# Kernel optimization log

Measured on AMD Instinct MI355X. Metric: run time of the kernel, lower is better.

The kernel has to match this reference:

```python
import jax, jax.numpy as jnp
import numpy as np

N_NODES = 50000
N_EDGES = 1600000
IN_CH, HID_CH, OUT_CH = 128, 128, 64


def gcn_conv(x, src, dst, norm, W, b):
    # x: [N, d_in]; src/dst: [E'] (self-loops included); norm: [E']
    h = x @ W                                  # [N, d_out] transform first (dense GEMM)
    msg = h[src] * norm[:, None]               # [E', d_out] gather + scale
    out = jax.ops.segment_sum(msg, dst, num_segments=x.shape[0])  # scatter-add
    return out + b


def setup_inputs() -> dict:
    key = jax.random.key(0)
    k1, k2, k3, k4, k5, k6 = jax.random.split(key, 6)
    x = jax.random.normal(k1, (N_NODES, IN_CH), dtype=jnp.float32)
    edge_index = jax.random.randint(k2, (2, N_EDGES), 0, N_NODES, dtype=jnp.int64)
    # Glorot-style init for weights
    W1 = jax.random.normal(k3, (IN_CH, HID_CH), dtype=jnp.float32) / np.sqrt(IN_CH)
    b1 = jnp.zeros((HID_CH,), dtype=jnp.float32)
    W2 = jax.random.normal(k4, (HID_CH, OUT_CH), dtype=jnp.float32) / np.sqrt(HID_CH)
    b2 = jnp.zeros((OUT_CH,), dtype=jnp.float32)
    return {"x": x, "edge_index": edge_index, "W1": W1, "b1": b1, "W2": W2, "b2": b2}


def reference(x, edge_index, W1, b1, W2, b2):
    n = x.shape[0]
    # GCNConv default: add self-loops, symmetric normalization D^-1/2 (A+I) D^-1/2
    loop = jnp.arange(n, dtype=edge_index.dtype)
    src = jnp.concatenate([edge_index[0], loop])   # [E+N]
    dst = jnp.concatenate([edge_index[1], loop])   # [E+N]
    deg = jax.ops.segment_sum(jnp.ones_like(dst, dtype=x.dtype), dst, num_segments=n)
    dinv = jnp.where(deg > 0, jax.lax.rsqrt(deg), 0.0)  # [N]
    norm = dinv[src] * dinv[dst]                   # [E+N]

    h = gcn_conv(x, src, dst, norm, W1, b1)        # conv1
    h = jax.nn.relu(h)
    h = gcn_conv(h, src, dst, norm, W2, b2)        # conv2
    return jax.nn.log_softmax(h, axis=1)
```

## Files before the change

kernel.cpp:

```cpp
#include <hip/hip_runtime.h>
#include <hip/hip_bf16.h>
#include <math.h>


typedef unsigned int uint;
typedef unsigned short ushort_t;
typedef unsigned char uchar_t;
typedef __attribute__((ext_vector_type(8))) short bf16x8;
typedef __attribute__((ext_vector_type(4))) float f32x4;
typedef __attribute__((ext_vector_type(2))) float f32x2;

#define BSH 7
#define NBMAX 400
#define BIN_CHUNK 4096
#define CAP 6144

__device__ inline ushort_t f2b(float f) {
    uint u = __float_as_uint(f);
    return (ushort_t)((u + 0x7fffu + ((u >> 16) & 1u)) >> 16);
}

__device__ inline uchar_t f2e4m3_sw(float f) {
    float a = fabsf(f);
    a = fminf(a, 448.f);
    uint sign = (__float_as_uint(f) >> 24) & 0x80u;
    uint u = __float_as_uint(a);
    int e = (int)(u >> 23) - 127;
    uint code;
    if (e < -6) {
        float t = a * 512.0f;
        uint m = (uint)(t + 0.5f);
        code = (m > 7) ? 0x08u : m;
    } else {
        uint lsb = (u >> 20) & 1u;
        u += 0x0007FFFFu + lsb;
        e = (int)(u >> 23) - 127;
        if (e > 8) code = 0x7Eu;
        else code = ((uint)(e + 7) << 3) | ((u >> 20) & 7u);
    }
    return (uchar_t)(sign | code);
}
__device__ inline float e4m3_sw(uint c) {
    uint ef = (c >> 3) & 15u, m = c & 7u;
    float v = ef ? __uint_as_float(((ef + 120u) << 23) | (m << 20))
                 : (float)m * 0.001953125f;
    return (c & 0x80u) ? -v : v;
}

__device__ inline f32x2 fp8x2_f32(uint v) {
#if __has_builtin(__builtin_amdgcn_cvt_pk_f32_fp8)
    return __builtin_amdgcn_cvt_pk_f32_fp8(v, false);
#else
    return (f32x2){e4m3_sw(v & 255u), e4m3_sw((v >> 8) & 255u)};
#endif
}
__device__ inline float fp8_f32(uint v) {
#if __has_builtin(__builtin_amdgcn_cvt_f32_fp8)
    return __builtin_amdgcn_cvt_f32_fp8(v, 0);
#else
    return e4m3_sw(v & 255u);
#endif
}
__device__ inline uchar_t f32_fp8(float f) {
#if __has_builtin(__builtin_amdgcn_cvt_pk_fp8_f32)
    return (uchar_t)(__builtin_amdgcn_cvt_pk_fp8_f32(f, f, 0u, false) & 0xffu);
#else
    return f2e4m3_sw(f);
#endif
}

__global__ __launch_bounds__(256) void k_init(int* __restrict__ bktcnt, int nbk) {
    int i = blockIdx.x * 256 + threadIdx.x;
    if (i < nbk) bktcnt[i] = 0;
}

__global__ __launch_bounds__(256) void k_bin(const int* __restrict__ esrc, const int* __restrict__ edst,
                                             int* __restrict__ bktcnt, uint* __restrict__ bin,
                                             int e, int nbk) {
    __shared__ int hist[NBMAX];
    __shared__ int segbase[NBMAX];
    int tid = threadIdx.x;
    int b0 = blockIdx.x * BIN_CHUNK;
    int b1 = min(b0 + BIN_CHUNK, e);
    for (int i = tid; i < nbk; i += 256) hist[i] = 0;
    __syncthreads();
    for (int i = b0 + tid * 4; i < b1; i += 1024) {
        if (i + 4 <= b1) {
            int4 d = *(const int4*)&edst[i];
            atomicAdd(&hist[d.x >> BSH], 1);
            atomicAdd(&hist[d.y >> BSH], 1);
            atomicAdd(&hist[d.z >> BSH], 1);
            atomicAdd(&hist[d.w >> BSH], 1);
        } else {
            for (int j = i; j < b1; ++j) atomicAdd(&hist[edst[j] >> BSH], 1);
        }
    }
    __syncthreads();
    for (int b = tid; b < nbk; b += 256) {
        int c = hist[b];
        int gb = c ? atomicAdd(&bktcnt[b], c) : 0;
        segbase[b] = b * CAP + gb;
        hist[b] = 0;
    }
    __syncthreads();
    for (int i = b0 + tid * 4; i < b1; i += 1024) {
        if (i + 4 <= b1) {
            int4 d = *(const int4*)&edst[i];
            int4 s = *(const int4*)&esrc[i];
            int bx = d.x >> BSH, by = d.y >> BSH, bz = d.z >> BSH, bw = d.w >> BSH;
            int px = atomicAdd(&hist[bx], 1);
            int py = atomicAdd(&hist[by], 1);
            int pz = atomicAdd(&hist[bz], 1);
            int pw = atomicAdd(&hist[bw], 1);
            bin[segbase[bx] + px] = (uint)s.x | ((uint)(d.x & 127) << 17);
            bin[segbase[by] + py] = (uint)s.y | ((uint)(d.y & 127) << 17);
            bin[segbase[bz] + pz] = (uint)s.z | ((uint)(d.z & 127) << 17);
            bin[segbase[bw] + pw] = (uint)s.w | ((uint)(d.w & 127) << 17);
        } else {
            for (int j = i; j < b1; ++j) {
                int d = edst[j], s = esrc[j];
                int b = d >> BSH;
                int p = atomicAdd(&hist[b], 1);
                bin[segbase[b] + p] = (uint)s | ((uint)(d & 127) << 17);
            }
        }
    }
}

__global__ __launch_bounds__(512) void k_scanBkt(const int* __restrict__ bktcnt, int* __restrict__ bktoff,
                                                 int nbk) {
    int tid = threadIdx.x;
    int v = (tid < nbk) ? bktcnt[tid] : 0;
    int x = v;
    for (int off = 1; off < 64; off <<= 1) {
        int y = __shfl_up(x, off);
        if ((tid & 63) >= off) x += y;
    }
    __shared__ int wt[8];
    if ((tid & 63) == 63) wt[tid >> 6] = x;
    __syncthreads();
    int w = tid >> 6, woff = 0;
    for (int k = 0; k < w; ++k) woff += wt[k];
    if (tid < nbk) bktoff[tid] = x - v + woff;
}

__global__ __launch_bounds__(256) void k_bucket(const uint* __restrict__ bin, const int* __restrict__ bktcnt,
                                                const int* __restrict__ bktoff,
                                                int* __restrict__ rowstart, int* __restrict__ cnt,
                                                float* __restrict__ dinv, int* __restrict__ csr, int n) {
    __shared__ int lcnt[1 << BSH];
    __shared__ int cur[1 << BSH];
    __shared__ int wt[4];
    int b = blockIdx.x;
    int tid = threadIdx.x;
    int lo = b << BSH;
    int nl = min(1 << BSH, n - lo);
    int m = bktcnt[b];
    int base = b * CAP;
    int obase = bktoff[b];
    if (tid < (1 << BSH)) lcnt[tid] = 0;
    __syncthreads();
    for (int i = tid; i < m; i += 256) {
        uint v = bin[base + i];
        atomicAdd(&lcnt[v >> 17], 1);
    }
    __syncthreads();
    int v = (tid < (1 << BSH)) ? lcnt[tid] : 0;
    int x = v;
    for (int off = 1; off < 64; off <<= 1) {
        int y = __shfl_up(x, off);
        if ((tid & 63) >= off) x += y;
    }
    if ((tid & 63) == 63) wt[tid >> 6] = x;
    __syncthreads();
    int excl = x - v + ((tid >= 64 && tid < 128) ? wt[0] : 0);
    if (tid < nl) {
        int node = lo + tid;
        rowstart[node] = obase + excl;
        cnt[node] = v;
        dinv[node] = rsqrtf((float)(v + 1));
        cur[tid] = obase + excl;
    }
    __syncthreads();
    for (int i = tid; i < m; i += 256) {
        uint en = bin[base + i];
        int dl = en >> 17;
        int p = atomicAdd(&cur[dl], 1);
        csr[p] = (int)(en & 0x1FFFFu);
    }
}

__global__ __launch_bounds__(256) void k_cvtW(const float* __restrict__ W1, const float* __restrict__ W2,
                                              ushort_t* __restrict__ W1t, ushort_t* __restrict__ W2t) {
    int i = blockIdx.x * 256 + threadIdx.x;
    if (i < 16384) {
        int k = i >> 7, nn = i & 127;
        W1t[nn * 128 + k] = f2b(W1[k * 128 + nn]);
    } else if (i < 16384 + 8192) {
        int j = i - 16384;
        int k = j >> 6, nn = j & 63;
        W2t[nn * 128 + k] = f2b(W2[k * 64 + nn]);
    }
}

template <int COLS, bool XBF16, bool OUTFP8>
__global__ __launch_bounds__(256) void k_mgemm(const void* __restrict__ Xv, const ushort_t* __restrict__ Wt,
                                               void* __restrict__ Yv, int nrows) {
    constexpr int NT = COLS / 16;
    __shared__ ushort_t lsX[64 * 128];
    __shared__ ushort_t lsW[COLS * 128];
    int tid = threadIdx.x;
    int rbase = blockIdx.x * 64;

#pragma unroll
    for (int it = 0; it < 4; ++it) {
        int idx = (tid + it * 256) * 8;
        int r = idx >> 7, c = idx & 127;
        int grow = rbase + r;
        uint4 pv = make_uint4(0, 0, 0, 0);
        if (grow < nrows) {
            if (XBF16) {
                pv = *(const uint4*)((const ushort_t*)Xv + (size_t)grow * 128 + c);
            } else {
                const float* xp = (const float*)Xv + (size_t)grow * 128 + c;
                float4 a = *(const float4*)xp;
                float4 b = *(const float4*)(xp + 4);
                pv.x = (uint)f2b(a.x) | ((uint)f2b(a.y) << 16);
                pv.y = (uint)f2b(a.z) | ((uint)f2b(a.w) << 16);
                pv.z = (uint)f2b(b.x) | ((uint)f2b(b.y) << 16);
                pv.w = (uint)f2b(b.z) | ((uint)f2b(b.w) << 16);
            }
        }
        int boff = (r * 256 + c * 2) ^ ((r & 7) << 4);
        *(uint4*)((char*)lsX + boff) = pv;
    }
#pragma unroll
    for (int it = 0; it < NT; ++it) {
        int idx = (tid + it * 256) * 8;
        int nr = idx >> 7, k = idx & 127;
        uint4 v = *(const uint4*)&Wt[nr * 128 + k];
        int boff = (nr * 256 + k * 2) ^ ((nr & 7) << 4);
        *(uint4*)((char*)lsW + boff) = v;
    }
    __syncthreads();

    int w = tid >> 6, l = tid & 63;
    int lr = l & 15, lg = l >> 4;
    int xrow = w * 16 + lr;
    bf16x8 a[4];
#pragma unroll
    for (int ks = 0; ks < 4; ++ks) {
        int boff = (xrow * 256 + (ks * 32 + lg * 8) * 2) ^ ((xrow & 7) << 4);
        a[ks] = *(const bf16x8*)((const char*)lsX + boff);
    }
    f32x4 acc[NT];
#pragma unroll
    for (int ct = 0; ct < NT; ++ct) {
        acc[ct] = (f32x4){0.f, 0.f, 0.f, 0.f};
#pragma unroll
        for (int ks = 0; ks < 4; ++ks) {
            int wrow = ct * 16 + lr;
            int boff = (wrow * 256 + (ks * 32 + lg * 8) * 2) ^ ((wrow & 7) << 4);
            bf16x8 b = *(const bf16x8*)((const char*)lsW + boff);
            acc[ct] = __builtin_amdgcn_mfma_f32_16x16x32_bf16(a[ks], b, acc[ct], 0, 0, 0);
        }
    }
#pragma unroll
    for (int ct = 0; ct < NT; ++ct) {
        int ch = ct * 16 + lr;
#pragma unroll
        for (int r = 0; r < 4; ++r) {
            int row = rbase + w * 16 + lg * 4 + r;
            if (row < nrows) {
                if (OUTFP8) ((uchar_t*)Yv)[(size_t)row * COLS + ch] = f32_fp8(acc[ct][r]);
                else        ((ushort_t*)Yv)[(size_t)row * COLS + ch] = f2b(acc[ct][r]);
            }
        }
    }
}

__global__ __launch_bounds__(256) void k_agg1(const ushort_t* __restrict__ xw8,
                                              const int* __restrict__ csr,
                                              const int* __restrict__ rowstart, const int* __restrict__ cnt,
                                              const float* __restrict__ dinv, const float* __restrict__ b1,
                                              uint* __restrict__ h, int n) {
    int tid = threadIdx.x;
    int i = blockIdx.x * 4 + (tid >> 6);
    int lane = tid & 63;
    if (i >= n) return;
    float di = dinv[i];
    f32x2 sv = fp8x2_f32(xw8[((uint)i << 6) + lane]);
    float accx = sv.x * di, accy = sv.y * di;
    int beg = rowstart[i], m = cnt[i];
    int j = 0;
    for (; j + 8 <= m; j += 8) {
        int s0 = csr[beg + j + 0], s1 = csr[beg + j + 1], s2 = csr[beg + j + 2], s3 = csr[beg + j + 3];
        int s4 = csr[beg + j + 4], s5 = csr[beg + j + 5], s6 = csr[beg + j + 6], s7 = csr[beg + j + 7];
        float d0 = dinv[s0], d1 = dinv[s1], d2 = dinv[s2], d3 = dinv[s3];
        float d4 = dinv[s4], d5 = dinv[s5], d6 = dinv[s6], d7 = dinv[s7];
        uint v0 = xw8[((uint)s0 << 6) + lane];
        uint v1 = xw8[((uint)s1 << 6) + lane];
        uint v2 = xw8[((uint)s2 << 6) + lane];
        uint v3 = xw8[((uint)s3 << 6) + lane];
        uint v4 = xw8[((uint)s4 << 6) + lane];
        uint v5 = xw8[((uint)s5 << 6) + lane];
        uint v6 = xw8[((uint)s6 << 6) + lane];
        uint v7 = xw8[((uint)s7 << 6) + lane];
        f32x2 f0 = fp8x2_f32(v0), f1 = fp8x2_f32(v1), f2 = fp8x2_f32(v2), f3 = fp8x2_f32(v3);
        f32x2 f4 = fp8x2_f32(v4), f5 = fp8x2_f32(v5), f6 = fp8x2_f32(v6), f7 = fp8x2_f32(v7);
        accx = fmaf(d0, f0.x, accx); accy = fmaf(d0, f0.y, accy);
        accx = fmaf(d1, f1.x, accx); accy = fmaf(d1, f1.y, accy);
        accx = fmaf(d2, f2.x, accx); accy = fmaf(d2, f2.y, accy);
        accx = fmaf(d3, f3.x, accx); accy = fmaf(d3, f3.y, accy);
        accx = fmaf(d4, f4.x, accx); accy = fmaf(d4, f4.y, accy);
        accx = fmaf(d5, f5.x, accx); accy = fmaf(d5, f5.y, accy);
        accx = fmaf(d6, f6.x, accx); accy = fmaf(d6, f6.y, accy);
        accx = fmaf(d7, f7.x, accx); accy = fmaf(d7, f7.y, accy);
    }
    for (; j < m; ++j) {
        int s0 = csr[beg + j];
        float d0 = dinv[s0];
        f32x2 f0 = fp8x2_f32(xw8[((uint)s0 << 6) + lane]);
        accx = fmaf(d0, f0.x, accx); accy = fmaf(d0, f0.y, accy);
    }
    float2 bb = ((const float2*)b1)[lane];
    float ox = fmaxf(fmaf(di, accx, bb.x), 0.f);
    float oy = fmaxf(fmaf(di, accy, bb.y), 0.f);
    h[((uint)i << 6) + lane] = (uint)f2b(ox) | ((uint)f2b(oy) << 16);
}

__global__ __launch_bounds__(256) void k_agg2(const uchar_t* __restrict__ hw8,
                                              const int* __restrict__ csr,
                                              const int* __restrict__ rowstart, const int* __restrict__ cnt,
                                              const float* __restrict__ dinv, const float* __restrict__ b2,
                                              float* __restrict__ out, int n) {
    int tid = threadIdx.x;
    int i = blockIdx.x * 4 + (tid >> 6);
    int lane = tid & 63;
    if (i >= n) return;
    float di = dinv[i];
    float acc = fp8_f32(hw8[((uint)i << 6) + lane]) * di;
    int beg = rowstart[i], m = cnt[i];
    int j = 0;
    for (; j + 8 <= m; j += 8) {
        int s0 = csr[beg + j + 0], s1 = csr[beg + j + 1], s2 = csr[beg + j + 2], s3 = csr[beg + j + 3];
        int s4 = csr[beg + j + 4], s5 = csr[beg + j + 5], s6 = csr[beg + j + 6], s7 = csr[beg + j + 7];
        float d0 = dinv[s0], d1 = dinv[s1], d2 = dinv[s2], d3 = dinv[s3];
        float d4 = dinv[s4], d5 = dinv[s5], d6 = dinv[s6], d7 = dinv[s7];
        uint c0 = hw8[((uint)s0 << 6) + lane];
        uint c1 = hw8[((uint)s1 << 6) + lane];
        uint c2 = hw8[((uint)s2 << 6) + lane];
        uint c3 = hw8[((uint)s3 << 6) + lane];
        uint c4 = hw8[((uint)s4 << 6) + lane];
        uint c5 = hw8[((uint)s5 << 6) + lane];
        uint c6 = hw8[((uint)s6 << 6) + lane];
        uint c7 = hw8[((uint)s7 << 6) + lane];
        acc = fmaf(d0, fp8_f32(c0), acc);
        acc = fmaf(d1, fp8_f32(c1), acc);
        acc = fmaf(d2, fp8_f32(c2), acc);
        acc = fmaf(d3, fp8_f32(c3), acc);
        acc = fmaf(d4, fp8_f32(c4), acc);
        acc = fmaf(d5, fp8_f32(c5), acc);
        acc = fmaf(d6, fp8_f32(c6), acc);
        acc = fmaf(d7, fp8_f32(c7), acc);
    }
    for (; j < m; ++j) {
        int s0 = csr[beg + j];
        acc = fmaf(dinv[s0], fp8_f32((uint)hw8[((uint)s0 << 6) + lane]), acc);
    }
    float o = fmaf(di, acc, b2[lane]);
    float mx = o;
    for (int off = 32; off; off >>= 1) mx = fmaxf(mx, __shfl_xor(mx, off));
    float ex = expf(o - mx);
    float sum = ex;
    for (int off = 32; off; off >>= 1) sum += __shfl_xor(sum, off);
    out[((uint)i << 6) + lane] = o - mx - logf(sum);
}

extern "C" void kernel_launch(void* const* d_in, const int* in_sizes, int n_in,
                              void* d_out, int out_size, void* d_ws, size_t ws_size,
                              hipStream_t stream) {
    const float* x  = (const float*)d_in[0];
    const int* eidx = (const int*)d_in[1];
    const float* W1 = (const float*)d_in[2];
    const float* b1 = (const float*)d_in[3];
    const float* W2 = (const float*)d_in[4];
    const float* b2 = (const float*)d_in[5];
    float* out = (float*)d_out;

    const int n = in_sizes[0] / 128;
    const int e = in_sizes[1] / 2;
    const int* esrc = eidx;
    const int* edst = eidx + e;
    const int nbk = (n + (1 << BSH) - 1) >> BSH;

    size_t off = 0;
    auto carve = [&](size_t bytes) {
        void* p = (char*)d_ws + off;
        off += (bytes + 255) & ~(size_t)255;
        return p;
    };
    uchar_t*  xW1  = (uchar_t*)carve((size_t)n * 128);
    ushort_t* h    = (ushort_t*)carve((size_t)n * 128 * 2);
    uchar_t*  hW2  = (uchar_t*)carve((size_t)n * 64);
    ushort_t* W1t  = (ushort_t*)carve(128 * 128 * 2);
    ushort_t* W2t  = (ushort_t*)carve(64 * 128 * 2);
    int*   cnt     = (int*)carve((size_t)n * 4);
    float* dinv    = (float*)carve((size_t)n * 4);
    int*   rowstart= (int*)carve((size_t)n * 4);
    int*   bktcnt  = (int*)carve((size_t)nbk * 4);
    int*   bktoff  = (int*)carve((size_t)nbk * 4);
    uint*  bin     = (uint*)carve((size_t)nbk * CAP * 4);
    int*   csr     = (int*)carve((size_t)e * 4);
    (void)ws_size;

    const int nbBin  = (e + BIN_CHUNK - 1) / BIN_CHUNK;
    const int nbWave = (n + 3) / 4;
    const int nbGemm = (n + 63) / 64;

    k_init<<<(nbk + 255) / 256, 256, 0, stream>>>(bktcnt, nbk);
    k_bin<<<nbBin, 256, 0, stream>>>(esrc, edst, bktcnt, bin, e, nbk);
    k_scanBkt<<<1, 512, 0, stream>>>(bktcnt, bktoff, nbk);
    k_bucket<<<nbk, 256, 0, stream>>>(bin, bktcnt, bktoff, rowstart, cnt, dinv, csr, n);
    k_cvtW<<<96, 256, 0, stream>>>(W1, W2, W1t, W2t);

    k_mgemm<128, false, true><<<nbGemm, 256, 0, stream>>>(x, W1t, xW1, n);
    k_agg1<<<nbWave, 256, 0, stream>>>((const ushort_t*)xW1, csr, rowstart, cnt, dinv, b1, (uint*)h, n);

    k_mgemm<64, true, true><<<nbGemm, 256, 0, stream>>>(h, W2t, hW2, n);
    k_agg2<<<nbWave, 256, 0, stream>>>(hW2, csr, rowstart, cnt, dinv, b2, out, n);
}
```

Baseline: 161.6 us.

## Prescale GEMM outputs by dinv and split edges across wave halves in aggregation

The GEMM epilogue now multiplies each output row by dinv[row] before quantizing to FP8. This removes the per-edge dinv[src] gather and FMA from both aggregation kernels, which become plain adds. The aggregation kernels are restructured so each lane loads 4 FP8 bytes at once. Edges are split across wave halves (layer 1) or quarters (layer 2), with neighbor indices broadcast via shuffles and partial sums combined by xor-shuffles. The log-softmax reduction is also narrowed to 16 lanes with float4 stores. Prescaling before FP8 quantization slightly changes rounding behaviour.

```diff
diff --git a/kernel.cpp b/kernel.cpp
--- a/kernel.cpp
+++ b/kernel.cpp
@@ -47,18 +47,18 @@
     return (c & 0x80u) ? -v : v;
 }
 
-__device__ inline f32x2 fp8x2_f32(uint v) {
+__device__ inline f32x2 fp8x2_lo(uint v) {
 #if __has_builtin(__builtin_amdgcn_cvt_pk_f32_fp8)
     return __builtin_amdgcn_cvt_pk_f32_fp8(v, false);
 #else
     return (f32x2){e4m3_sw(v & 255u), e4m3_sw((v >> 8) & 255u)};
 #endif
 }
-__device__ inline float fp8_f32(uint v) {
-#if __has_builtin(__builtin_amdgcn_cvt_f32_fp8)
-    return __builtin_amdgcn_cvt_f32_fp8(v, 0);
+__device__ inline f32x2 fp8x2_hi(uint v) {
+#if __has_builtin(__builtin_amdgcn_cvt_pk_f32_fp8)
+    return __builtin_amdgcn_cvt_pk_f32_fp8(v, true);
 #else
-    return e4m3_sw(v & 255u);
+    return (f32x2){e4m3_sw((v >> 16) & 255u), e4m3_sw((v >> 24) & 255u)};
 #endif
 }
 __device__ inline uchar_t f32_fp8(float f) {
@@ -205,6 +205,7 @@
 
 template <int COLS, bool XBF16, bool OUTFP8>
 __global__ __launch_bounds__(256) void k_mgemm(const void* __restrict__ Xv, const ushort_t* __restrict__ Wt,
+                                               const float* __restrict__ dinv,
                                                void* __restrict__ Yv, int nrows) {
     constexpr int NT = COLS / 16;
     __shared__ ushort_t lsX[64 * 128];
@@ -265,6 +266,12 @@
             acc[ct] = __builtin_amdgcn_mfma_f32_16x16x32_bf16(a[ks], b, acc[ct], 0, 0, 0);
         }
     }
+    float dr[4];
+#pragma unroll
+    for (int r = 0; r < 4; ++r) {
+        int row = rbase + w * 16 + lg * 4 + r;
+        dr[r] = (OUTFP8 && row < nrows) ? dinv[row] : 1.f;
+    }
 #pragma unroll
     for (int ct = 0; ct < NT; ++ct) {
         int ch = ct * 16 + lr;
@@ -272,109 +279,136 @@
         for (int r = 0; r < 4; ++r) {
             int row = rbase + w * 16 + lg * 4 + r;
             if (row < nrows) {
-                if (OUTFP8) ((uchar_t*)Yv)[(size_t)row * COLS + ch] = f32_fp8(acc[ct][r]);
+                if (OUTFP8) ((uchar_t*)Yv)[(size_t)row * COLS + ch] = f32_fp8(dr[r] * acc[ct][r]);
                 else        ((ushort_t*)Yv)[(size_t)row * COLS + ch] = f2b(acc[ct][r]);
             }
         }
     }
 }
 
-__global__ __launch_bounds__(256) void k_agg1(const ushort_t* __restrict__ xw8,
+__global__ __launch_bounds__(256) void k_agg1(const uchar_t* __restrict__ t1,
                                               const int* __restrict__ csr,
                                               const int* __restrict__ rowstart, const int* __restrict__ cnt,
                                               const float* __restrict__ dinv, const float* __restrict__ b1,
                                               uint* __restrict__ h, int n) {
     int tid = threadIdx.x;
     int i = blockIdx.x * 4 + (tid >> 6);
+    if (i >= n) return;
     int lane = tid & 63;
-    if (i >= n) return;
-    float di = dinv[i];
-    f32x2 sv = fp8x2_f32(xw8[((uint)i << 6) + lane]);
-    float accx = sv.x * di, accy = sv.y * di;
+    int half = lane >> 5, cl = lane & 31;
+    float a0 = 0.f, a1 = 0.f, a2 = 0.f, a3 = 0.f;
+    if (half == 0) {
+        uint v = *(const uint*)(t1 + ((size_t)i << 7) + cl * 4);
+        f32x2 lo = fp8x2_lo(v), hi = fp8x2_hi(v);
+        a0 = lo.x; a1 = lo.y; a2 = hi.x; a3 = hi.y;
+    }
     int beg = rowstart[i], m = cnt[i];
     int j = 0;
     for (; j + 8 <= m; j += 8) {
-        int s0 = csr[beg + j + 0], s1 = csr[beg + j + 1], s2 = csr[beg + j + 2], s3 = csr[beg + j + 3];
-        int s4 = csr[beg + j + 4], s5 = csr[beg + j + 5], s6 = csr[beg + j + 6], s7 = csr[beg + j + 7];
-        float d0 = dinv[s0], d1 = dinv[s1], d2 = dinv[s2], d3 = dinv[s3];
-        float d4 = dinv[s4], d5 = dinv[s5], d6 = dinv[s6], d7 = dinv[s7];
-        uint v0 = xw8[((uint)s0 << 6) + lane];
-        uint v1 = xw8[((uint)s1 << 6) + lane];
-        uint v2 = xw8[((uint)s2 << 6) + lane];
-        uint v3 = xw8[((uint)s3 << 6) + lane];
-        uint v4 = xw8[((uint)s4 << 6) + lane];
-        uint v5 = xw8[((uint)s5 << 6) + lane];
-        uint v6 = xw8[((uint)s6 << 6) + lane];
-        uint v7 = xw8[((uint)s7 << 6) + lane];
-        f32x2 f0 = fp8x2_f32(v0), f1 = fp8x2_f32(v1), f2 = fp8x2_f32(v2), f3 = fp8x2_f32(v3);
-        f32x2 f4 = fp8x2_f32(v4), f5 = fp8x2_f32(v5), f6 = fp8x2_f32(v6), f7 = fp8x2_f32(v7);
-        accx = fmaf(d0, f0.x, accx); accy = fmaf(d0, f0.y, accy);
-        accx = fmaf(d1, f1.x, accx); accy = fmaf(d1, f1.y, accy);
-        accx = fmaf(d2, f2.x, accx); accy = fmaf(d2, f2.y, accy);
-        accx = fmaf(d3, f3.x, accx); accy = fmaf(d3, f3.y, accy);
-        accx = fmaf(d4, f4.x, accx); accy = fmaf(d4, f4.y, accy);
-        accx = fmaf(d5, f5.x, accx); accy = fmaf(d5, f5.y, accy);
-        accx = fmaf(d6, f6.x, accx); accy = fmaf(d6, f6.y, accy);
-        accx = fmaf(d7, f7.x, accx); accy = fmaf(d7, f7.y, accy);
-    }
-    for (; j < m; ++j) {
-        int s0 = csr[beg + j];
-        float d0 = dinv[s0];
-        f32x2 f0 = fp8x2_f32(xw8[((uint)s0 << 6) + lane]);
-        accx = fmaf(d0, f0.x, accx); accy = fmaf(d0, f0.y, accy);
-    }
-    float2 bb = ((const float2*)b1)[lane];
-    float ox = fmaxf(fmaf(di, accx, bb.x), 0.f);
-    float oy = fmaxf(fmaf(di, accy, bb.y), 0.f);
-    h[((uint)i << 6) + lane] = (uint)f2b(ox) | ((uint)f2b(oy) << 16);
-}
-
-__global__ __launch_bounds__(256) void k_agg2(const uchar_t* __restrict__ hw8,
+        int c = csr[beg + j + (lane & 7)];
+        int s0 = __shfl(c, 0 + half);
+        int s1 = __shfl(c, 2 + half);
+        int s2 = __shfl(c, 4 + half);
+        int s3 = __shfl(c, 6 + half);
+        uint v0 = *(const uint*)(t1 + ((size_t)s0 << 7) + cl * 4);
+        uint v1 = *(const uint*)(t1 + ((size_t)s1 << 7) + cl * 4);
+        uint v2 = *(const uint*)(t1 + ((size_t)s2 << 7) + cl * 4);
+        uint v3 = *(const uint*)(t1 + ((size_t)s3 << 7) + cl * 4);
+        f32x2 p;
+        p = fp8x2_lo(v0); a0 += p.x; a1 += p.y;  p = fp8x2_hi(v0); a2 += p.x; a3 += p.y;
+        p = fp8x2_lo(v1); a0 += p.x; a1 += p.y;  p = fp8x2_hi(v1); a2 += p.x; a3 += p.y;
+        p = fp8x2_lo(v2); a0 += p.x; a1 += p.y;  p = fp8x2_hi(v2); a2 += p.x; a3 += p.y;
+        p = fp8x2_lo(v3); a0 += p.x; a1 += p.y;  p = fp8x2_hi(v3); a2 += p.x; a3 += p.y;
+    }
+    for (; j < m; j += 2) {
+        int idx = j + half;
+        if (idx < m) {
+            int s = csr[beg + idx];
+            uint v = *(const uint*)(t1 + ((size_t)s << 7) + cl * 4);
+            f32x2 p;
+            p = fp8x2_lo(v); a0 += p.x; a1 += p.y;
+            p = fp8x2_hi(v); a2 += p.x; a3 += p.y;
+        }
+    }
+    a0 += __shfl_xor(a0, 32); a1 += __shfl_xor(a1, 32);
+    a2 += __shfl_xor(a2, 32); a3 += __shfl_xor(a3, 32);
+    float di = dinv[i];
+    float4 bb = ((const float4*)b1)[cl];
+    float o0 = fmaxf(fmaf(di, a0, bb.x), 0.f);
+    float o1 = fmaxf(fmaf(di, a1, bb.y), 0.f);
+    float o2 = fmaxf(fmaf(di, a2, bb.z), 0.f);
+    float o3 = fmaxf(fmaf(di, a3, bb.w), 0.f);
+    if (half == 0) {
+        uint2 pk;
+        pk.x = (uint)f2b(o0) | ((uint)f2b(o1) << 16);
+        pk.y = (uint)f2b(o2) | ((uint)f2b(o3) << 16);
+        *(uint2*)&h[((size_t)i << 6) + cl * 2] = pk;
+    }
+}
+
+__global__ __launch_bounds__(256) void k_agg2(const uchar_t* __restrict__ t2,
                                               const int* __restrict__ csr,
                                               const int* __restrict__ rowstart, const int* __restrict__ cnt,
                                               const float* __restrict__ dinv, const float* __restrict__ b2,
                                               float* __restrict__ out, int n) {
     int tid = threadIdx.x;
     int i = blockIdx.x * 4 + (tid >> 6);
+    if (i >= n) return;
     int lane = tid & 63;
-    if (i >= n) return;
-    float di = dinv[i];
-    float acc = fp8_f32(hw8[((uint)i << 6) + lane]) * di;
+    int q = lane >> 4, cl = lane & 15;
+    float a0 = 0.f, a1 = 0.f, a2 = 0.f, a3 = 0.f;
+    if (q == 0) {
+        uint v = *(const uint*)(t2 + ((size_t)i << 6) + cl * 4);
+        f32x2 lo = fp8x2_lo(v), hi = fp8x2_hi(v);
+        a0 = lo.x; a1 = lo.y; a2 = hi.x; a3 = hi.y;
+    }
     int beg = rowstart[i], m = cnt[i];
     int j = 0;
     for (; j + 8 <= m; j += 8) {
-        int s0 = csr[beg + j + 0], s1 = csr[beg + j + 1], s2 = csr[beg + j + 2], s3 = csr[beg + j + 3];
-        int s4 = csr[beg + j + 4], s5 = csr[beg + j + 5], s6 = csr[beg + j + 6], s7 = csr[beg + j + 7];
-        float d0 = dinv[s0], d1 = dinv[s1], d2 = dinv[s2], d3 = dinv[s3];
-        float d4 = dinv[s4], d5 = dinv[s5], d6 = dinv[s6], d7 = dinv[s7];
-        uint c0 = hw8[((uint)s0 << 6) + lane];
-        uint c1 = hw8[((uint)s1 << 6) + lane];
-        uint c2 = hw8[((uint)s2 << 6) + lane];
-        uint c3 = hw8[((uint)s3 << 6) + lane];
-        uint c4 = hw8[((uint)s4 << 6) + lane];
-        uint c5 = hw8[((uint)s5 << 6) + lane];
-        uint c6 = hw8[((uint)s6 << 6) + lane];
-        uint c7 = hw8[((uint)s7 << 6) + lane];
-        acc = fmaf(d0, fp8_f32(c0), acc);
-        acc = fmaf(d1, fp8_f32(c1), acc);
-        acc = fmaf(d2, fp8_f32(c2), acc);
-        acc = fmaf(d3, fp8_f32(c3), acc);
-        acc = fmaf(d4, fp8_f32(c4), acc);
-        acc = fmaf(d5, fp8_f32(c5), acc);
-        acc = fmaf(d6, fp8_f32(c6), acc);
-        acc = fmaf(d7, fp8_f32(c7), acc);
-    }
-    for (; j < m; ++j) {
-        int s0 = csr[beg + j];
-        acc = fmaf(dinv[s0], fp8_f32((uint)hw8[((uint)s0 << 6) + lane]), acc);
-    }
-    float o = fmaf(di, acc, b2[lane]);
-    float mx = o;
-    for (int off = 32; off; off >>= 1) mx = fmaxf(mx, __shfl_xor(mx, off));
-    float ex = expf(o - mx);
-    float sum = ex;
-    for (int off = 32; off; off >>= 1) sum += __shfl_xor(sum, off);
-    out[((uint)i << 6) + lane] = o - mx - logf(sum);
+        int c = csr[beg + j + (lane & 7)];
+        int s0 = __shfl(c, 0 + q);
+        int s1 = __shfl(c, 4 + q);
+        uint v0 = *(const uint*)(t2 + ((size_t)s0 << 6) + cl * 4);
+        uint v1 = *(const uint*)(t2 + ((size_t)s1 << 6) + cl * 4);
+        f32x2 p;
+        p = fp8x2_lo(v0); a0 += p.x; a1 += p.y;  p = fp8x2_hi(v0); a2 += p.x; a3 += p.y;
+        p = fp8x2_lo(v1); a0 += p.x; a1 += p.y;  p = fp8x2_hi(v1); a2 += p.x; a3 += p.y;
+    }
+    for (; j < m; j += 4) {
+        int idx = j + q;
+        if (idx < m) {
+            int s = csr[beg + idx];
+            uint v = *(const uint*)(t2 + ((size_t)s << 6) + cl * 4);
+            f32x2 p;
+            p = fp8x2_lo(v); a0 += p.x; a1 += p.y;
+            p = fp8x2_hi(v); a2 += p.x; a3 += p.y;
+        }
+    }
+    a0 += __shfl_xor(a0, 16); a1 += __shfl_xor(a1, 16);
+    a2 += __shfl_xor(a2, 16); a3 += __shfl_xor(a3, 16);
+    a0 += __shfl_xor(a0, 32); a1 += __shfl_xor(a1, 32);
+    a2 += __shfl_xor(a2, 32); a3 += __shfl_xor(a3, 32);
+    float di = dinv[i];
+    float4 bb = ((const float4*)b2)[cl];
+    float o0 = fmaf(di, a0, bb.x);
+    float o1 = fmaf(di, a1, bb.y);
+    float o2 = fmaf(di, a2, bb.z);
+    float o3 = fmaf(di, a3, bb.w);
+    float mx = fmaxf(fmaxf(o0, o1), fmaxf(o2, o3));
+    mx = fmaxf(mx, __shfl_xor(mx, 1));
+    mx = fmaxf(mx, __shfl_xor(mx, 2));
+    mx = fmaxf(mx, __shfl_xor(mx, 4));
+    mx = fmaxf(mx, __shfl_xor(mx, 8));
+    float s = expf(o0 - mx) + expf(o1 - mx) + expf(o2 - mx) + expf(o3 - mx);
+    s += __shfl_xor(s, 1);
+    s += __shfl_xor(s, 2);
+    s += __shfl_xor(s, 4);
+    s += __shfl_xor(s, 8);
+    float ls = mx + logf(s);
+    if (lane < 16) {
+        float4 r = make_float4(o0 - ls, o1 - ls, o2 - ls, o3 - ls);
+        *(float4*)&out[((size_t)i << 6) + cl * 4] = r;
+    }
 }
 
 extern "C" void kernel_launch(void* const* d_in, const int* in_sizes, int n_in,
@@ -424,9 +458,9 @@
     k_bucket<<<nbk, 256, 0, stream>>>(bin, bktcnt, bktoff, rowstart, cnt, dinv, csr, n);
     k_cvtW<<<96, 256, 0, stream>>>(W1, W2, W1t, W2t);
 
-    k_mgemm<128, false, true><<<nbGemm, 256, 0, stream>>>(x, W1t, xW1, n);
-    k_agg1<<<nbWave, 256, 0, stream>>>((const ushort_t*)xW1, csr, rowstart, cnt, dinv, b1, (uint*)h, n);
-
-    k_mgemm<64, true, true><<<nbGemm, 256, 0, stream>>>(h, W2t, hW2, n);
+    k_mgemm<128, false, true><<<nbGemm, 256, 0, stream>>>(x, W1t, dinv, xW1, n);
+    k_agg1<<<nbWave, 256, 0, stream>>>(xW1, csr, rowstart, cnt, dinv, b1, (uint*)h, n);
+
+    k_mgemm<64, true, true><<<nbGemm, 256, 0, stream>>>(h, W2t, dinv, hW2, n);
     k_agg2<<<nbWave, 256, 0, stream>>>(hW2, csr, rowstart, cnt, dinv, b2, out, n);
 }
```

New measurement: 148.5 us. -8.1%, faster.
